# Kernel optimization log

Hardware: AMD Instinct MI355X
Metric: run time of the kernel (lower is better)

Reference implementation:

```python
import jax, jax.numpy as jnp
import numpy as np

B, T, D, H = 2, 2048, 2048, 32
d = D // H  # head_dim = 64


def setup_inputs() -> dict:
    key = jax.random.key(0)
    ks = jax.random.split(key, 6)
    s = 2 ** (-2.5) * (2.0 / (D + D)) ** 0.5  # xavier_uniform-ish scale, gain 2^-2.5
    return {
        "hidden_states": jax.random.normal(ks[0], (B, T, D), jnp.float32),
        "Wq": jax.random.normal(ks[1], (D, D), jnp.float32) * s,
        "Wk": jax.random.normal(ks[2], (D, D), jnp.float32) * s,
        "Wv": jax.random.normal(ks[3], (D, D), jnp.float32) * s,
        "Wbeta": jax.random.normal(ks[4], (D, H), jnp.float32) * s,
        "b_beta": jnp.zeros((H,), jnp.float32),
        "Wo": jax.random.normal(ks[5], (D, D), jnp.float32) * s,
    }


def _l2norm(x):
    return x * jax.lax.rsqrt(jnp.sum(x * x, axis=-1, keepdims=True) + 1e-6)


def _parallel_hope(q, k, v, beta):
    """Householder delta-rule linear attention.
    q,k,v: [B,H,T,d]; beta: [B,H,T].
    Recurrence: S_t = S_{t-1} (I - beta_t k_t k_t^T) + beta_t k_t v_t^T  (k l2-normalized,
    so the update is a generalized Householder transform), o_t = q_t^T S_t.
    """
    q = _l2norm(q)
    k = _l2norm(k)

    def step(S, inp):
        q_t, k_t, v_t, b_t = inp  # [B,H,d], [B,H,d], [B,H,d], [B,H]
        # delta rule: new value replaces old prediction, gated by beta
        pred = jnp.einsum('bhk,bhkv->bhv', k_t, S)
        delta = (v_t - pred) * b_t[..., None]
        S = S + jnp.einsum('bhk,bhv->bhkv', k_t, delta)
        o_t = jnp.einsum('bhk,bhkv->bhv', q_t, S)
        return S, o_t

    S0 = jnp.zeros(q.shape[:2] + (q.shape[-1], v.shape[-1]), q.dtype)  # [B,H,d,d]
    xs = (jnp.moveaxis(q, 2, 0), jnp.moveaxis(k, 2, 0),
          jnp.moveaxis(v, 2, 0), jnp.moveaxis(beta, 2, 0))
    _, o = jax.lax.scan(step, S0, xs)  # [T,B,H,d]
    return jnp.moveaxis(o, 0, 2)  # [B,H,T,d]


def reference(hidden_states, Wq, Wk, Wv, Wbeta, b_beta, Wo):
    q = hidden_states @ Wq
    k = hidden_states @ Wk
    v = hidden_states @ Wv
    beta = jax.nn.sigmoid(hidden_states @ Wbeta + b_beta)  # [B,T,H]
    to_heads = lambda x: jnp.moveaxis(x.reshape(B, T, H, d), 1, 2)  # [B,H,T,d]
    q, k, v = to_heads(q), to_heads(k), to_heads(v)
    beta = jnp.moveaxis(beta, 1, 2)  # [B,H,T]
    o = _parallel_hope(q, k, v, beta)  # [B,H,T,d]
    o = jnp.moveaxis(o, 1, 2).reshape(B, T, D)
    return o @ Wo
```

## Files before the change

### kernel.cpp

```cpp
#include <hip/hip_runtime.h>
#include <hip/hip_bf16.h>

typedef __hip_bfloat16 bf16;
typedef __attribute__((ext_vector_type(8))) short short8;
typedef __attribute__((ext_vector_type(4))) float f32x4;

#define NB 2
#define NT 2048
#define ND 2048
#define NH 32
#define NM (NB*NT)
#define NCH 32

__global__ void detect_dtype(const unsigned short* __restrict__ hs, int* __restrict__ flag) {
  if (threadIdx.x == 0 && blockIdx.x == 0) {
    int cnt = 0;
    for (int i = 0; i < 2048; i += 2) {
      int e = (hs[i] >> 7) & 0xFF;
      if (e >= 141) ++cnt;
    }
    *flag = (cnt > 64) ? 1 : 0;
  }
}

__device__ __forceinline__ float loadf(const void* p, size_t i, int isf32) {
  return isf32 ? ((const float*)p)[i] : __bfloat162float(((const bf16*)p)[i]);
}

__global__ __launch_bounds__(256) void convert_bf16(const void* __restrict__ src,
                                                    bf16* __restrict__ dst,
                                                    long n, const int* __restrict__ flag) {
  const long i0 = ((long)blockIdx.x * 256 + threadIdx.x) * 8;
  if (i0 >= n) return;
  if (*flag) {
    const float* s = (const float*)src;
    #pragma unroll
    for (int j = 0; j < 8; ++j) dst[i0 + j] = __float2bfloat16(s[i0 + j]);
  } else {
    *(short8*)(dst + i0) = *(const short8*)((const bf16*)src + i0);
  }
}

__global__ __launch_bounds__(256) void transpose_cvt(const void* __restrict__ src,
                                                     bf16* __restrict__ dst,
                                                     int src_rows, int src_cols,
                                                     const int* __restrict__ flag) {
  __shared__ bf16 tile[64][65];
  const int f = *flag;
  const int tb_r = blockIdx.y * 64, tb_c = blockIdx.x * 64;
  const int tx = threadIdx.x & 63, ty = threadIdx.x >> 6;
  #pragma unroll
  for (int i = 0; i < 64; i += 4) {
    const int cc = tb_c + tx;
    tile[i + ty][tx] = (cc < src_cols)
      ? __float2bfloat16(loadf(src, (size_t)(tb_r + i + ty) * src_cols + cc, f))
      : __float2bfloat16(0.f);
  }
  __syncthreads();
  #pragma unroll
  for (int i = 0; i < 64; i += 4)
    dst[(size_t)(tb_c + i + ty) * src_rows + tb_r + tx] = tile[tx][i + ty];
}

__global__ __launch_bounds__(256) void transpose_qkvb(const void* __restrict__ Wq,
                                                      const void* __restrict__ Wk,
                                                      const void* __restrict__ Wv,
                                                      const void* __restrict__ Wb,
                                                      bf16* __restrict__ WT,
                                                      const int* __restrict__ flag) {
  __shared__ bf16 tile[64][65];
  const int z = blockIdx.z;
  if (z == 3 && blockIdx.x >= 4) return;
  const void* src = (z == 0) ? Wq : (z == 1) ? Wk : (z == 2) ? Wv : Wb;
  const int src_cols = (z == 3) ? 32 : 2048;
  bf16* dst = WT + (size_t)z * 2048 * 2048;
  const int f = *flag;
  const int tb_r = blockIdx.y * 64, tb_c = blockIdx.x * 64;
  const int tx = threadIdx.x & 63, ty = threadIdx.x >> 6;
  #pragma unroll
  for (int i = 0; i < 64; i += 4) {
    const int cc = tb_c + tx;
    tile[i + ty][tx] = (cc < src_cols)
      ? __float2bfloat16(loadf(src, (size_t)(tb_r + i + ty) * src_cols + cc, f))
      : __float2bfloat16(0.f);
  }
  __syncthreads();
  #pragma unroll
  for (int i = 0; i < 64; i += 4)
    dst[(size_t)(tb_c + i + ty) * 2048 + tb_r + tx] = tile[tx][i + ty];
}

__device__ __forceinline__ void gload_lds16(const void* g, void* l) {
  __builtin_amdgcn_global_load_lds((__attribute__((address_space(1))) const void*)g,
                                   (__attribute__((address_space(3))) void*)l,
                                   16, 0, 0);
}

__global__ __launch_bounds__(256) void gemm_bt(const bf16* __restrict__ A,
                                               const bf16* __restrict__ Bt,
                                               bf16* __restrict__ oq, bf16* __restrict__ ok2,
                                               bf16* __restrict__ ov, bf16* __restrict__ ob,
                                               void* __restrict__ outv,
                                               const int* __restrict__ outflag,
                                               int M, int K, int n_base) {
  __shared__ bf16 As[128 * 32];
  __shared__ bf16 Bs[128 * 32];
  const int tid = threadIdx.x;
  const int wave = tid >> 6, lane = tid & 63;
  const int m0 = blockIdx.y * 128, n0 = blockIdx.x * 128;
  const int wm = (wave >> 1) * 64, wn = (wave & 1) * 64;
  const int srow = lane >> 2, scol = (lane & 3) * 8;
  const int frow = lane & 15, fk = (lane >> 4) * 8;
  f32x4 acc[4][4] = {};

  for (int kb = 0; kb < K; kb += 32) {
    __syncthreads();
    #pragma unroll
    for (int j = 0; j < 2; ++j) {
      const int rbase = wave * 32 + j * 16;
      gload_lds16(A  + (size_t)(m0 + rbase + srow) * K + kb + scol, As + rbase * 32);
      gload_lds16(Bt + (size_t)(n0 + rbase + srow) * K + kb + scol, Bs + rbase * 32);
    }
    __syncthreads();
    short8 af[4], bfr[4];
    #pragma unroll
    for (int i = 0; i < 4; ++i)
      af[i] = *(const short8*)(As + (wm + i * 16 + frow) * 32 + fk);
    #pragma unroll
    for (int i = 0; i < 4; ++i)
      bfr[i] = *(const short8*)(Bs + (wn + i * 16 + frow) * 32 + fk);
    #pragma unroll
    for (int mi = 0; mi < 4; ++mi)
      #pragma unroll
      for (int ni = 0; ni < 4; ++ni)
        acc[mi][ni] = __builtin_amdgcn_mfma_f32_16x16x32_bf16(af[mi], bfr[ni], acc[mi][ni], 0, 0, 0);
  }

  const int crow = (lane >> 4) * 4, ccol = lane & 15;
  const int gn0 = n_base + n0;
  if (outflag) {
    const int f = *outflag;
    #pragma unroll
    for (int mi = 0; mi < 4; ++mi)
      #pragma unroll
      for (int ni = 0; ni < 4; ++ni)
        #pragma unroll
        for (int r = 0; r < 4; ++r) {
          const size_t idx = (size_t)(m0 + wm + mi * 16 + crow + r) * 2048 + gn0 + wn + ni * 16 + ccol;
          const float val = acc[mi][ni][r];
          if (f == 1) ((float*)outv)[idx] = val;
          else        ((bf16*)outv)[idx] = __float2bfloat16(val);
        }
  } else {
    const int seg = gn0 >> 11;
    bf16* o = (seg == 0) ? oq : (seg == 1) ? ok2 : (seg == 2) ? ov : ob;
    const int stride = (seg < 3) ? 2048 : 128;
    const int cb = (gn0 & 2047) + wn;
    if (seg <= 1) {
      #pragma unroll
      for (int mi = 0; mi < 4; ++mi)
        #pragma unroll
        for (int r = 0; r < 4; ++r) {
          float s = acc[mi][0][r] * acc[mi][0][r] + acc[mi][1][r] * acc[mi][1][r]
                  + acc[mi][2][r] * acc[mi][2][r] + acc[mi][3][r] * acc[mi][3][r];
          s += __shfl_xor(s, 1, 64); s += __shfl_xor(s, 2, 64);
          s += __shfl_xor(s, 4, 64); s += __shfl_xor(s, 8, 64);
          const float inv = rsqrtf(s + 1e-6f);
          #pragma unroll
          for (int ni = 0; ni < 4; ++ni) acc[mi][ni][r] *= inv;
        }
    }
    #pragma unroll
    for (int mi = 0; mi < 4; ++mi)
      #pragma unroll
      for (int ni = 0; ni < 4; ++ni)
        #pragma unroll
        for (int r = 0; r < 4; ++r)
          o[(size_t)(m0 + wm + mi * 16 + crow + r) * stride + cb + ni * 16 + ccol] =
            __float2bfloat16(acc[mi][ni][r]);
  }
}


#define MFMA_PAIR(P)                                                             \
  _Pragma("unroll") for (int q2 = 0; q2 < 2; ++q2)                               \
    _Pragma("unroll") for (int ni2 = 0; ni2 < 4; ++ni2) {                        \
      acc[(P) * 2 + q2][ni2] = __builtin_amdgcn_mfma_f32_16x16x32_bf16(          \
          aF[q2][0], bF[ni2][0], acc[(P) * 2 + q2][ni2], 0, 0, 0);               \
      acc[(P) * 2 + q2][ni2] = __builtin_amdgcn_mfma_f32_16x16x32_bf16(          \
          aF[q2][1], bF[ni2][1], acc[(P) * 2 + q2][ni2], 0, 0, 0);               \
    }

#define READ_A(P)                                                                \
  _Pragma("unroll") for (int q2 = 0; q2 < 2; ++q2)                               \
    _Pragma("unroll") for (int kk = 0; kk < 2; ++kk)                             \
      aF[q2][kk] = *(const short8*)(lA + (((P) * 2 + q2) * 16 + frow) * 128      \
                                       + ((kk * 64 + fq * 16) ^ fswz));

#define READ_B_ALL()                                                             \
  _Pragma("unroll") for (int ni2 = 0; ni2 < 4; ++ni2)                            \
    _Pragma("unroll") for (int kk = 0; kk < 2; ++kk)                             \
      bF[ni2][kk] = *(const short8*)(lB + (brow0 + ni2 * 16 + frow) * 128        \
                                        + ((kk * 64 + fq * 16) ^ fswz));

#define PH_OPEN() do { __builtin_amdgcn_s_barrier();                             \
  asm volatile("s_waitcnt lgkmcnt(0)" ::: "memory");                             \
  __builtin_amdgcn_sched_barrier(0);                                             \
  __builtin_amdgcn_s_setprio(1); } while (0)

#define PH_CLOSE() do { __builtin_amdgcn_s_setprio(0);                           \
  __builtin_amdgcn_s_barrier(); } while (0)

__global__ __launch_bounds__(512, 2) void gemm256(const bf16* __restrict__ A,
                                                  const bf16* __restrict__ Bt,
                                                  bf16* __restrict__ oq, bf16* __restrict__ ok2,
                                                  bf16* __restrict__ ov, bf16* __restrict__ ob,
                                                  void* __restrict__ outv,
                                                  const int* __restrict__ outflag,
                                                  int K, int ntn) {
  __shared__ bf16 LA[2][2][8192];
  __shared__ bf16 LB[2][2][8192];
  const int tid = threadIdx.x;
  const int wave = tid >> 6, lane = tid & 63;
  const int wm = wave >> 2, wn = wave & 3;
  const int frow = lane & 15, fq = lane >> 4;
  const int cpx = (int)gridDim.x >> 3;
  const int wg = ((int)blockIdx.x & 7) * cpx + ((int)blockIdx.x >> 3);
  const int mtile = wg / ntn, ntile = wg % ntn;
  const int m0 = mtile * 256, n0 = ntile * 256;
  const int NTK = K >> 6;
  const int fswz = (frow & 7) << 4;
  int srow[2], scolb[2];
  #pragma unroll
  for (int j = 0; j < 2; ++j) {
    const int q = wave * 1024 + j * 8192 + lane * 16;
    const int qs = q ^ (((q >> 7) & 7) << 4);
    srow[j]  = qs >> 7;
    scolb[j] = (qs & 127) >> 1;
  }
  const int lofs = wave * 1024;

  f32x4 acc[8][4] = {};

  auto STAGE = [&](const bf16* __restrict__ G, int row0, int kcol, bf16* lhalf) {
    #pragma unroll
    for (int j = 0; j < 2; ++j)
      gload_lds16(G + (size_t)(row0 + srow[j]) * K + kcol + scolb[j],
                  (char*)lhalf + lofs + j * 8192);
  };

  STAGE(A,  m0,       0,  LA[0][0]);
  STAGE(A,  m0 + 128, 0,  LA[0][1]);
  STAGE(Bt, n0,       0,  LB[0][0]);
  STAGE(Bt, n0 + 128, 0,  LB[0][1]);
  STAGE(A,  m0,       64, LA[1][0]);
  STAGE(A,  m0 + 128, 64, LA[1][1]);
  asm volatile("s_waitcnt vmcnt(4)" ::: "memory");
  __builtin_amdgcn_s_barrier();

  const int brow0 = (wn & 1) * 64;
  #pragma unroll 1
  for (int t = 0; t < NTK; ++t) {
    const int par = t & 1;
    const char* lA = (const char*)LA[par][wm];
    const char* lB = (const char*)LB[par][wn >> 1];
    short8 aF[2][2], bF[4][2];
    READ_A(0)
    READ_B_ALL()
    if (t + 1 < NTK) STAGE(Bt, n0, (t + 1) * 64, LB[par ^ 1][0]);
    PH_OPEN();
    MFMA_PAIR(0)
    PH_CLOSE();
    READ_A(1)
    if (t + 1 < NTK) STAGE(Bt, n0 + 128, (t + 1) * 64, LB[par ^ 1][1]);
    PH_OPEN();
    MFMA_PAIR(1)
    PH_CLOSE();
    READ_A(2)
    PH_OPEN();
    MFMA_PAIR(2)
    PH_CLOSE();
    READ_A(3)
    PH_OPEN();
    MFMA_PAIR(3)
    __builtin_amdgcn_s_setprio(0);
    __builtin_amdgcn_s_barrier();
    if (t + 1 < NTK) {
      if (t + 2 < NTK) {
        STAGE(A, m0,       (t + 2) * 64, LA[par][0]);
        STAGE(A, m0 + 128, (t + 2) * 64, LA[par][1]);
      }
      if (t == NTK - 2) asm volatile("s_waitcnt vmcnt(0)" ::: "memory");
      else              asm volatile("s_waitcnt vmcnt(4)" ::: "memory");
      __builtin_amdgcn_s_barrier();
    }
  }

  const int crow = fq * 4, ccol = frow;
  const int rowb = m0 + wm * 128;
  if (outv) {
    const int f = *outflag;
    const int cb = n0 + wn * 64;
    #pragma unroll
    for (int mi = 0; mi < 8; ++mi)
      #pragma unroll
      for (int ni = 0; ni < 4; ++ni)
        #pragma unroll
        for (int r = 0; r < 4; ++r) {
          const size_t idx = (size_t)(rowb + mi * 16 + crow + r) * 2048 + cb + ni * 16 + ccol;
          const float val = acc[mi][ni][r];
          if (f == 1) ((float*)outv)[idx] = val;
          else        ((bf16*)outv)[idx] = __float2bfloat16(val);
        }
    return;
  }
  const int gn0w = n0 + wn * 64;
  const int seg = gn0w >> 11;
  bf16* o = (seg == 0) ? oq : (seg == 1) ? ok2 : (seg == 2) ? ov : ob;
  const int stride = (seg < 3) ? 2048 : 256;
  const int cb = (seg < 3) ? (gn0w & 2047) : (gn0w - 6144);
  if (seg <= 1) {
    #pragma unroll
    for (int mi = 0; mi < 8; ++mi)
      #pragma unroll
      for (int r = 0; r < 4; ++r) {
        float s = acc[mi][0][r] * acc[mi][0][r] + acc[mi][1][r] * acc[mi][1][r]
                + acc[mi][2][r] * acc[mi][2][r] + acc[mi][3][r] * acc[mi][3][r];
        s += __shfl_xor(s, 1, 64); s += __shfl_xor(s, 2, 64);
        s += __shfl_xor(s, 4, 64); s += __shfl_xor(s, 8, 64);
        const float inv = rsqrtf(s + 1e-6f);
        #pragma unroll
        for (int ni = 0; ni < 4; ++ni) acc[mi][ni][r] *= inv;
      }
  }
  #pragma unroll
  for (int mi = 0; mi < 8; ++mi)
    #pragma unroll
    for (int ni = 0; ni < 4; ++ni)
      #pragma unroll
      for (int r = 0; r < 4; ++r)
        o[(size_t)(rowb + mi * 16 + crow + r) * stride + cb + ni * 16 + ccol] =
          __float2bfloat16(acc[mi][ni][r]);
}


template<int TB>
__device__ __forceinline__ void scan16(const float* __restrict__ Af,
                                       const bf16* __restrict__ vsrc,
                                       const float* __restrict__ Bsc,
                                       float (&u)[64], const int lane, const int wave,
                                       const float sgn,
                                       bf16* __restrict__ outT,
                                       bf16* __restrict__ gout) {
  constexpr int JM = (TB + 1) * 16;
  #pragma unroll
  for (int tt = 0; tt < 16; ++tt) {
    const int t = TB * 16 + tt;
    float pr0 = 0.f, pr1 = 0.f, pr2 = 0.f, pr3 = 0.f;
    #pragma unroll
    for (int i = 0; i < JM; i += 4) {
      const f32x4 a = *(const f32x4*)(Af + t * 64 + i);
      pr0 = __builtin_fmaf(a[0], u[i + 0], pr0);
      pr1 = __builtin_fmaf(a[1], u[i + 1], pr1);
      pr2 = __builtin_fmaf(a[2], u[i + 2], pr2);
      pr3 = __builtin_fmaf(a[3], u[i + 3], pr3);
    }
    const float ut = Bsc[t] * __bfloat162float(vsrc[t * 72 + lane])
                   - ((pr0 + pr1) + (pr2 + pr3));
    u[t] = ut;
    const bf16 sv = __float2bfloat16(sgn * ut);
    outT[lane * 72 + t] = sv;
    if (wave) gout[t * 64 + lane] = sv;
  }
}

__global__ __launch_bounds__(256) void chunk_scan(const bf16* __restrict__ k16,
                                                  bf16* __restrict__ v16,
                                                  const bf16* __restrict__ betab,
                                                  const void* __restrict__ bb,
                                                  const int* __restrict__ flag,
                                                  bf16* __restrict__ Gneg,
                                                  bf16* __restrict__ AcT,
                                                  bf16* __restrict__ Dc) {
  __shared__ bf16 Ks[64 * 72];
  __shared__ bf16 Vs[64 * 72];
  __shared__ bf16 GsT[64 * 72];
  __shared__ bf16 UsT[64 * 72];
  __shared__ float Af[64 * 64];
  __shared__ float Bsc[64];
  bf16* const KTs = (bf16*)Af;
  const int ch = blockIdx.x;
  const int c = ch & (NCH - 1), bh = ch >> 5;
  const int h = bh & (NH - 1), b = bh >> 5;
  const int tid = threadIdx.x, wave = tid >> 6, lane = tid & 63;
  const size_t rowb = ((size_t)b * NT + c * 64) * ND + (size_t)h * 64;

  short8 ktA0, ktB0, ktA1, ktB1;
  if (wave >= 2) {
    const int d0a = (wave - 2) * 16, d0b = d0a + 32;
    ktA0 = *(const short8*)(k16 + rowb + (size_t)lane * ND + d0a);
    ktB0 = *(const short8*)(k16 + rowb + (size_t)lane * ND + d0a + 8);
    ktA1 = *(const short8*)(k16 + rowb + (size_t)lane * ND + d0b);
    ktB1 = *(const short8*)(k16 + rowb + (size_t)lane * ND + d0b + 8);
  }
  {
    const int r0 = tid >> 3, sc = (tid & 7) * 8;
    #pragma unroll
    for (int rnd = 0; rnd < 2; ++rnd) {
      const int r = rnd * 32 + r0;
      *(short8*)(Ks + r * 72 + sc) = *(const short8*)(k16 + rowb + (size_t)r * ND + sc);
      *(short8*)(Vs + r * 72 + sc) = *(const short8*)(v16 + rowb + (size_t)r * ND + sc);
    }
  }
  if (tid < 64) {
    const float x = __bfloat162float(betab[((size_t)b * NT + c * 64 + tid) * 256 + h])
                    + loadf(bb, h, *flag);
    Bsc[tid] = 1.f / (1.f + expf(-x));
  }
  __syncthreads();

  const int frow = lane & 15, fk = (lane >> 4) * 8, cm = (lane >> 4) * 4;
  {
    short8 ma0 = *(const short8*)(Ks + (16 * wave + frow) * 72 + fk);
    short8 ma1 = *(const short8*)(Ks + (16 * wave + frow) * 72 + 32 + fk);
    #pragma unroll
    for (int n = 0; n < 4; ++n) {
      f32x4 m = {};
      m = __builtin_amdgcn_mfma_f32_16x16x32_bf16(ma0, *(const short8*)(Ks + (16 * n + frow) * 72 + fk), m, 0, 0, 0);
      m = __builtin_amdgcn_mfma_f32_16x16x32_bf16(ma1, *(const short8*)(Ks + (16 * n + frow) * 72 + 32 + fk), m, 0, 0, 0);
      #pragma unroll
      for (int r = 0; r < 4; ++r) {
        const int t = 16 * wave + cm + r, s = 16 * n + frow;
        Af[t * 64 + s] = (s < t) ? Bsc[t] * m[r] : 0.f;
      }
    }
  }
  __syncthreads();

  if (wave < 2) {
    float u[64];
    #pragma unroll
    for (int i = 0; i < 64; ++i) u[i] = 0.f;
    const bf16* vsrc = wave ? Ks : Vs;
    bf16* outT = wave ? GsT : UsT;
    bf16* gout = Gneg + (size_t)ch * 4096;
    const float sgn = wave ? -1.f : 1.f;
    scan16<0>(Af, vsrc, Bsc, u, lane, wave, sgn, outT, gout);
    scan16<1>(Af, vsrc, Bsc, u, lane, wave, sgn, outT, gout);
    scan16<2>(Af, vsrc, Bsc, u, lane, wave, sgn, outT, gout);
    scan16<3>(Af, vsrc, Bsc, u, lane, wave, sgn, outT, gout);
  }
  __syncthreads();

  if (wave >= 2) {
    const int d0a = (wave - 2) * 16, d0b = d0a + 32;
    #pragma unroll
    for (int j = 0; j < 8; ++j) {
      KTs[(d0a + j) * 72 + lane]     = ((const bf16*)&ktA0)[j];
      KTs[(d0a + 8 + j) * 72 + lane] = ((const bf16*)&ktB0)[j];
      KTs[(d0b + j) * 72 + lane]     = ((const bf16*)&ktA1)[j];
      KTs[(d0b + 8 + j) * 72 + lane] = ((const bf16*)&ktB1)[j];
    }
  }
  __syncthreads();

  short8 ka0 = *(const short8*)(KTs + (16 * wave + frow) * 72 + fk);
  short8 ka1 = *(const short8*)(KTs + (16 * wave + frow) * 72 + 32 + fk);
  short8 uu0 = *(const short8*)(UsT + (16 * wave + frow) * 72 + fk);
  short8 uu1 = *(const short8*)(UsT + (16 * wave + frow) * 72 + 32 + fk);
  #pragma unroll
  for (int n = 0; n < 4; ++n) {
    f32x4 aA = {}, aD = {};
    aA = __builtin_amdgcn_mfma_f32_16x16x32_bf16(ka0, *(const short8*)(GsT + (16 * n + frow) * 72 + fk), aA, 0, 0, 0);
    aA = __builtin_amdgcn_mfma_f32_16x16x32_bf16(ka1, *(const short8*)(GsT + (16 * n + frow) * 72 + 32 + fk), aA, 0, 0, 0);
    aD = __builtin_amdgcn_mfma_f32_16x16x32_bf16(uu0, *(const short8*)(KTs + (16 * n + frow) * 72 + fk), aD, 0, 0, 0);
    aD = __builtin_amdgcn_mfma_f32_16x16x32_bf16(uu1, *(const short8*)(KTs + (16 * n + frow) * 72 + 32 + fk), aD, 0, 0, 0);
    #pragma unroll
    for (int r = 0; r < 4; ++r) {
      Vs[(16 * wave + cm + r) * 64 + 16 * n + frow] = __float2bfloat16(aA[r]);
      Ks[(16 * wave + cm + r) * 64 + 16 * n + frow] = __float2bfloat16(aD[r]);
    }
  }
  __syncthreads();
  {
    const int r0 = tid >> 2, sc2 = (tid & 3) * 16;
    bf16* acg = AcT + (size_t)ch * 4096;
    bf16* dcg = Dc  + (size_t)ch * 4096;
    *(short8*)(acg + r0 * 64 + sc2)     = *(const short8*)(Vs + r0 * 64 + sc2);
    *(short8*)(acg + r0 * 64 + sc2 + 8) = *(const short8*)(Vs + r0 * 64 + sc2 + 8);
    *(short8*)(dcg + r0 * 64 + sc2)     = *(const short8*)(Ks + r0 * 64 + sc2);
    *(short8*)(dcg + r0 * 64 + sc2 + 8) = *(const short8*)(Ks + r0 * 64 + sc2 + 8);
    *(short8*)(v16 + rowb + (size_t)r0 * ND + sc2)     = *(const short8*)(UsT + r0 * 72 + sc2);
    *(short8*)(v16 + rowb + (size_t)r0 * ND + sc2 + 8) = *(const short8*)(UsT + r0 * 72 + sc2 + 8);
  }
}

__global__ __launch_bounds__(256) void state_seq(const bf16* __restrict__ AcT,
                                                 const bf16* __restrict__ Dc,
                                                 bf16* __restrict__ Sbuf) {
  __shared__ bf16 ST[64 * 72];
  const int bh = blockIdx.x;
  const int wave = threadIdx.x >> 6, lane = threadIdx.x & 63;
  const int frow = lane & 15, fk = (lane >> 4) * 8, cm = (lane >> 4) * 4;
  for (int i = threadIdx.x; i < 64 * 72 / 2; i += 256) ((unsigned int*)ST)[i] = 0u;
  f32x4 sacc[4] = {};
  const bf16* ac = AcT + (size_t)bh * NCH * 4096;
  const bf16* dc = Dc  + (size_t)bh * NCH * 4096;
  bf16* sb = Sbuf + (size_t)bh * NCH * 4096;
  #pragma unroll
  for (int n = 0; n < 4; ++n)
    #pragma unroll
    for (int r = 0; r < 4; ++r)
      sb[(16 * wave + cm + r) * 64 + 16 * n + frow] = __float2bfloat16(0.f);
  short8 bpre[4][2];
  float dpre[16];
  #pragma unroll
  for (int n = 0; n < 4; ++n) {
    bpre[n][0] = *(const short8*)(ac + (16 * n + frow) * 64 + fk);
    bpre[n][1] = *(const short8*)(ac + (16 * n + frow) * 64 + 32 + fk);
    #pragma unroll
    for (int r = 0; r < 4; ++r)
      dpre[n * 4 + r] = __bfloat162float(dc[(16 * wave + cm + r) * 64 + 16 * n + frow]);
  }
  __syncthreads();
  #pragma unroll 1
  for (int c = 0; c < NCH; ++c) {
    short8 a0 = *(const short8*)(ST + (16 * wave + frow) * 72 + fk);
    short8 a1 = *(const short8*)(ST + (16 * wave + frow) * 72 + 32 + fk);
    short8 bcur[4][2];
    float dcur[16];
    #pragma unroll
    for (int n = 0; n < 4; ++n) {
      bcur[n][0] = bpre[n][0]; bcur[n][1] = bpre[n][1];
      #pragma unroll
      for (int r = 0; r < 4; ++r) dcur[n * 4 + r] = dpre[n * 4 + r];
    }
    if (c + 1 < NCH) {
      const bf16* acn = ac + (size_t)(c + 1) * 4096;
      const bf16* dcn = dc + (size_t)(c + 1) * 4096;
      #pragma unroll
      for (int n = 0; n < 4; ++n) {
        bpre[n][0] = *(const short8*)(acn + (16 * n + frow) * 64 + fk);
        bpre[n][1] = *(const short8*)(acn + (16 * n + frow) * 64 + 32 + fk);
        #pragma unroll
        for (int r = 0; r < 4; ++r)
          dpre[n * 4 + r] = __bfloat162float(dcn[(16 * wave + cm + r) * 64 + 16 * n + frow]);
      }
    }
    #pragma unroll
    for (int n = 0; n < 4; ++n) {
      sacc[n] = __builtin_amdgcn_mfma_f32_16x16x32_bf16(a0, bcur[n][0], sacc[n], 0, 0, 0);
      sacc[n] = __builtin_amdgcn_mfma_f32_16x16x32_bf16(a1, bcur[n][1], sacc[n], 0, 0, 0);
      #pragma unroll
      for (int r = 0; r < 4; ++r) sacc[n][r] += dcur[n * 4 + r];
    }
    __syncthreads();
    #pragma unroll
    for (int n = 0; n < 4; ++n)
      #pragma unroll
      for (int r = 0; r < 4; ++r) {
        const bf16 sv = __float2bfloat16(sacc[n][r]);
        ST[(16 * wave + cm + r) * 72 + 16 * n + frow] = sv;
        if (c + 1 < NCH)
          sb[(size_t)(c + 1) * 4096 + (16 * wave + cm + r) * 64 + 16 * n + frow] = sv;
      }
    __syncthreads();
  }
}

__global__ __launch_bounds__(256) void chunk_out(bf16* __restrict__ q16,
                                                 const bf16* __restrict__ k16,
                                                 const bf16* __restrict__ v16,
                                                 const bf16* __restrict__ Gneg,
                                                 const bf16* __restrict__ Sbuf) {
  __shared__ bf16 UTs[64 * 72];
  __shared__ bf16 Pt[64 * 72];
  const int ch = blockIdx.x;
  const int c = ch & (NCH - 1), bh = ch >> 5;
  const int h = bh & (NH - 1), b = bh >> 5;
  const int tid = threadIdx.x, wave = tid >> 6, lane = tid & 63;
  const int frow = lane & 15, fk = (lane >> 4) * 8, cm = (lane >> 4) * 4;
  const size_t qkb = ((size_t)b * NT + c * 64) * ND + (size_t)h * 64;
  const bf16* Sb = Sbuf + (size_t)ch * 4096;
  const bf16* Gc = Gneg + (size_t)ch * 4096;
  {
    const int r0 = tid >> 2, sc2 = (tid & 3) * 16;
    *(short8*)(UTs + r0 * 72 + sc2)     = *(const short8*)(v16 + qkb + (size_t)r0 * ND + sc2);
    *(short8*)(UTs + r0 * 72 + sc2 + 8) = *(const short8*)(v16 + qkb + (size_t)r0 * ND + sc2 + 8);
  }
  short8 qa0 = *(const short8*)(q16 + qkb + (size_t)(16 * wave + frow) * ND + fk);
  short8 qa1 = *(const short8*)(q16 + qkb + (size_t)(16 * wave + frow) * ND + 32 + fk);
  f32x4 pacc[4];
  #pragma unroll
  for (int n = 0; n < 4; ++n) {
    f32x4 a = {};
    a = __builtin_amdgcn_mfma_f32_16x16x32_bf16(qa0, *(const short8*)(k16 + qkb + (size_t)(16 * n + frow) * ND + fk), a, 0, 0, 0);
    a = __builtin_amdgcn_mfma_f32_16x16x32_bf16(qa1, *(const short8*)(k16 + qkb + (size_t)(16 * n + frow) * ND + 32 + fk), a, 0, 0, 0);
    pacc[n] = a;
  }
  __syncthreads();
  f32x4 uacc[4];
  #pragma unroll
  for (int n = 0; n < 4; ++n)
    #pragma unroll
    for (int r = 0; r < 4; ++r)
      uacc[n][r] = __bfloat162float(UTs[(16 * wave + cm + r) * 72 + 16 * n + frow]);
  #pragma unroll
  for (int n = 0; n < 4; ++n)
    #pragma unroll
    for (int r = 0; r < 4; ++r) {
      const int mg = 16 * wave + cm + r, ng = 16 * n + frow;
      Pt[mg * 72 + ng] = __float2bfloat16(ng <= mg ? pacc[n][r] : 0.f);
    }
  short8 sa0 = *(const short8*)(Sb + (16 * wave + frow) * 64 + fk);
  short8 sa1 = *(const short8*)(Sb + (16 * wave + frow) * 64 + 32 + fk);
  #pragma unroll
  for (int n = 0; n < 4; ++n) {
    uacc[n] = __builtin_amdgcn_mfma_f32_16x16x32_bf16(sa0, *(const short8*)(Gc + (16 * n + frow) * 64 + fk), uacc[n], 0, 0, 0);
    uacc[n] = __builtin_amdgcn_mfma_f32_16x16x32_bf16(sa1, *(const short8*)(Gc + (16 * n + frow) * 64 + 32 + fk), uacc[n], 0, 0, 0);
  }
  __syncthreads();
  #pragma unroll
  for (int n = 0; n < 4; ++n)
    #pragma unroll
    for (int r = 0; r < 4; ++r)
      UTs[(16 * wave + cm + r) * 72 + 16 * n + frow] = __float2bfloat16(uacc[n][r]);
  __syncthreads();
  short8 pa0 = *(const short8*)(Pt + (16 * wave + frow) * 72 + fk);
  short8 pa1 = *(const short8*)(Pt + (16 * wave + frow) * 72 + 32 + fk);
  #pragma unroll
  for (int n = 0; n < 4; ++n) {
    f32x4 o = {};
    o = __builtin_amdgcn_mfma_f32_16x16x32_bf16(qa0, *(const short8*)(Sb + (16 * n + frow) * 64 + fk), o, 0, 0, 0);
    o = __builtin_amdgcn_mfma_f32_16x16x32_bf16(qa1, *(const short8*)(Sb + (16 * n + frow) * 64 + 32 + fk), o, 0, 0, 0);
    o = __builtin_amdgcn_mfma_f32_16x16x32_bf16(pa0, *(const short8*)(UTs + (16 * n + frow) * 72 + fk), o, 0, 0, 0);
    o = __builtin_amdgcn_mfma_f32_16x16x32_bf16(pa1, *(const short8*)(UTs + (16 * n + frow) * 72 + 32 + fk), o, 0, 0, 0);
    #pragma unroll
    for (int r = 0; r < 4; ++r)
      q16[qkb + (size_t)(16 * wave + cm + r) * ND + 16 * n + frow] = __float2bfloat16(o[r]);
  }
}


__global__ __launch_bounds__(128) void chunk_scan_c(const bf16* __restrict__ k16,
                                                    bf16* __restrict__ v16,
                                                    const bf16* __restrict__ betab,
                                                    const void* __restrict__ bb,
                                                    const int* __restrict__ flag,
                                                    bf16* __restrict__ Gneg) {
  __shared__ bf16 Ks[64 * 64];
  __shared__ bf16 Vs[64 * 64];
  __shared__ bf16 Gs[64 * 64];
  __shared__ float Bs[64];
  const int ch = blockIdx.x;
  const int c = ch & (NCH - 1), bh = ch >> 5;
  const int h = bh & (NH - 1), b = bh >> 5;
  const int tid = threadIdx.x;
  const int wave = tid >> 6, lane = tid & 63;
  const size_t rowb = ((size_t)b * NT + c * 64) * ND + (size_t)h * 64;
  const int sr = tid >> 3, sc = (tid & 7) * 8;
  #pragma unroll
  for (int rnd = 0; rnd < 4; ++rnd) {
    const int r = rnd * 16 + sr;
    *(short8*)(Ks + r * 64 + sc) = *(const short8*)(k16 + rowb + (size_t)r * ND + sc);
    *(short8*)(Vs + r * 64 + sc) = *(const short8*)(v16 + rowb + (size_t)r * ND + sc);
  }
  if (tid < 64) {
    const float x = __bfloat162float(betab[((size_t)b * NT + c * 64 + tid) * 128 + h])
                    + loadf(bb, h, *flag);
    Bs[tid] = 1.f / (1.f + expf(-x));
  }
  __syncthreads();
  float S[64];
  #pragma unroll
  for (int i = 0; i < 64; ++i) S[i] = 0.f;
  const bf16* val_src = wave ? Ks : Vs;
  #pragma unroll 1
  for (int t = 0; t < 64; ++t) {
    uint4 ku[8];
    #pragma unroll
    for (int i = 0; i < 8; ++i) ku[i] = ((const uint4*)(Ks + t * 64))[i];
    const float val = __bfloat162float(val_src[t * 64 + lane]);
    const float bt = Bs[t];
    float kvf[64];
    #pragma unroll
    for (int i = 0; i < 8; ++i) {
      kvf[8*i+0] = __uint_as_float(ku[i].x << 16);
      kvf[8*i+1] = __uint_as_float(ku[i].x & 0xffff0000u);
      kvf[8*i+2] = __uint_as_float(ku[i].y << 16);
      kvf[8*i+3] = __uint_as_float(ku[i].y & 0xffff0000u);
      kvf[8*i+4] = __uint_as_float(ku[i].z << 16);
      kvf[8*i+5] = __uint_as_float(ku[i].z & 0xffff0000u);
      kvf[8*i+6] = __uint_as_float(ku[i].w << 16);
      kvf[8*i+7] = __uint_as_float(ku[i].w & 0xffff0000u);
    }
    float p0 = 0, p1 = 0, p2 = 0, p3 = 0;
    #pragma unroll
    for (int i = 0; i < 16; ++i) {
      p0 += kvf[4*i+0] * S[4*i+0];
      p1 += kvf[4*i+1] * S[4*i+1];
      p2 += kvf[4*i+2] * S[4*i+2];
      p3 += kvf[4*i+3] * S[4*i+3];
    }
    const float u = bt * (val - ((p0 + p1) + (p2 + p3)));
    #pragma unroll
    for (int i = 0; i < 16; ++i) {
      S[4*i+0] += kvf[4*i+0] * u;
      S[4*i+1] += kvf[4*i+1] * u;
      S[4*i+2] += kvf[4*i+2] * u;
      S[4*i+3] += kvf[4*i+3] * u;
    }
    if (wave) Gs[t * 64 + lane] = __float2bfloat16(-u);
    else      Vs[t * 64 + lane] = __float2bfloat16(u);
  }
  __syncthreads();
  bf16* gout = Gneg + (size_t)ch * 4096;
  #pragma unroll
  for (int rnd = 0; rnd < 4; ++rnd) {
    const int r = rnd * 16 + sr;
    *(short8*)(v16 + rowb + (size_t)r * ND + sc) = *(const short8*)(Vs + r * 64 + sc);
    *(short8*)(gout + r * 64 + sc)               = *(const short8*)(Gs + r * 64 + sc);
  }
}

__global__ __launch_bounds__(256) void chunk_seq_mono(bf16* q16,
                                                      const bf16* __restrict__ k16,
                                                      const bf16* __restrict__ Ul,
                                                      const bf16* __restrict__ Gneg) {
  __shared__ bf16 ST[64 * 72];
  __shared__ bf16 Ubt[64 * 72];
  __shared__ bf16 Pt[64 * 72];
  __shared__ bf16 KTl[64 * 72];
  const int bh = blockIdx.x, h = bh & (NH - 1), b = bh >> 5;
  const int wave = threadIdx.x >> 6, lane = threadIdx.x & 63;
  const int frow = lane & 15, q4 = lane >> 4, fk = q4 * 8;
  const int cm = q4 * 4;
  for (int i = threadIdx.x; i < 64 * 72 / 2; i += 256) ((unsigned int*)ST)[i] = 0u;
  __syncthreads();
  f32x4 sacc[4] = {};
  #pragma unroll 1
  for (int c = 0; c < NCH; ++c) {
    const bf16* Gc = Gneg + ((size_t)bh * NCH + c) * 4096;
    const size_t qkb = ((size_t)b * NT + c * 64) * ND + (size_t)h * 64;
    {
      short8 r0 = *(const short8*)(k16 + qkb + (size_t)lane * ND + 16 * wave);
      short8 r1 = *(const short8*)(k16 + qkb + (size_t)lane * ND + 16 * wave + 8);
      #pragma unroll
      for (int j = 0; j < 8; ++j) {
        KTl[(16 * wave + j) * 72 + lane]     = ((const bf16*)&r0)[j];
        KTl[(16 * wave + 8 + j) * 72 + lane] = ((const bf16*)&r1)[j];
      }
    }
    short8 ga0 = *(const short8*)(Gc + (16 * wave + frow) * 64 + fk);
    short8 ga1 = *(const short8*)(Gc + (16 * wave + frow) * 64 + 32 + fk);
    #pragma unroll
    for (int n = 0; n < 4; ++n) {
      f32x4 acc;
      #pragma unroll
      for (int r = 0; r < 4; ++r)
        acc[r] = __bfloat162float(Ul[qkb + (size_t)(16 * wave + cm + r) * ND + 16 * n + frow]);
      acc = __builtin_amdgcn_mfma_f32_16x16x32_bf16(ga0, *(const short8*)(ST + (16 * n + frow) * 72 + fk), acc, 0, 0, 0);
      acc = __builtin_amdgcn_mfma_f32_16x16x32_bf16(ga1, *(const short8*)(ST + (16 * n + frow) * 72 + 32 + fk), acc, 0, 0, 0);
      #pragma unroll
      for (int r = 0; r < 4; ++r)
        Ubt[(16 * n + frow) * 72 + 16 * wave + cm + r] = __float2bfloat16(acc[r]);
    }
    __syncthreads();
    short8 qa0 = *(const short8*)(q16 + qkb + (size_t)(16 * wave + frow) * ND + fk);
    short8 qa1 = *(const short8*)(q16 + qkb + (size_t)(16 * wave + frow) * ND + 32 + fk);
    #pragma unroll
    for (int n = 0; n < 4; ++n) {
      f32x4 acc = {};
      acc = __builtin_amdgcn_mfma_f32_16x16x32_bf16(qa0, *(const short8*)(k16 + qkb + (size_t)(16 * n + frow) * ND + fk), acc, 0, 0, 0);
      acc = __builtin_amdgcn_mfma_f32_16x16x32_bf16(qa1, *(const short8*)(k16 + qkb + (size_t)(16 * n + frow) * ND + 32 + fk), acc, 0, 0, 0);
      #pragma unroll
      for (int r = 0; r < 4; ++r) {
        const int mg = 16 * wave + cm + r, ng = 16 * n + frow;
        Pt[mg * 72 + ng] = __float2bfloat16(ng <= mg ? acc[r] : 0.f);
      }
    }
    __syncthreads();
    short8 pa0 = *(const short8*)(Pt + (16 * wave + frow) * 72 + fk);
    short8 pa1 = *(const short8*)(Pt + (16 * wave + frow) * 72 + 32 + fk);
    #pragma unroll
    for (int n = 0; n < 4; ++n) {
      f32x4 acc = {};
      acc = __builtin_amdgcn_mfma_f32_16x16x32_bf16(qa0, *(const short8*)(ST + (16 * n + frow) * 72 + fk), acc, 0, 0, 0);
      acc = __builtin_amdgcn_mfma_f32_16x16x32_bf16(qa1, *(const short8*)(ST + (16 * n + frow) * 72 + 32 + fk), acc, 0, 0, 0);
      acc = __builtin_amdgcn_mfma_f32_16x16x32_bf16(pa0, *(const short8*)(Ubt + (16 * n + frow) * 72 + fk), acc, 0, 0, 0);
      acc = __builtin_amdgcn_mfma_f32_16x16x32_bf16(pa1, *(const short8*)(Ubt + (16 * n + frow) * 72 + 32 + fk), acc, 0, 0, 0);
      #pragma unroll
      for (int r = 0; r < 4; ++r)
        q16[qkb + (size_t)(16 * wave + cm + r) * ND + 16 * n + frow] = __float2bfloat16(acc[r]);
    }
    __syncthreads();
    short8 ua0 = *(const short8*)(Ubt + (16 * wave + frow) * 72 + fk);
    short8 ua1 = *(const short8*)(Ubt + (16 * wave + frow) * 72 + 32 + fk);
    #pragma unroll
    for (int n = 0; n < 4; ++n) {
      sacc[n] = __builtin_amdgcn_mfma_f32_16x16x32_bf16(ua0, *(const short8*)(KTl + (16 * n + frow) * 72 + fk), sacc[n], 0, 0, 0);
      sacc[n] = __builtin_amdgcn_mfma_f32_16x16x32_bf16(ua1, *(const short8*)(KTl + (16 * n + frow) * 72 + 32 + fk), sacc[n], 0, 0, 0);
      #pragma unroll
      for (int r = 0; r < 4; ++r)
        ST[(16 * wave + cm + r) * 72 + 16 * n + frow] = __float2bfloat16(sacc[n][r]);
    }
    __syncthreads();
  }
}

extern "C" void kernel_launch(void* const* d_in, const int* in_sizes, int n_in,
                              void* d_out, int out_size, void* d_ws, size_t ws_size,
                              hipStream_t stream) {
  const void* hs = d_in[0];
  const void* Wq = d_in[1];
  const void* Wk = d_in[2];
  const void* Wv = d_in[3];
  const void* Wb = d_in[4];
  const void* bb = d_in[5];
  const void* Wo = d_in[6];

  char* ws = (char*)d_ws;
  size_t off = 0;
  auto alloc = [&](size_t bytes) {
    void* p = ws + off;
    off += (bytes + 255) & ~(size_t)255;
    return p;
  };
  const size_t szW2 = (size_t)32 * 1024 * 1024;
  const size_t szM  = (size_t)NM * ND * 2;
  const size_t szB2 = (size_t)NM * 256 * 2;
  const size_t szB  = (size_t)NM * 128 * 2;
  const size_t need_fused = 512 + szW2 + 4 * szM + szB2 + szM;

  if (ws_size >= need_fused) {
    int*  flag  = (int*) alloc(256);
    bf16* WT    = (bf16*)alloc(szW2);
    bf16* hs16  = (bf16*)alloc(szM);
    bf16* q16   = (bf16*)alloc(szM);
    bf16* k16   = (bf16*)alloc(szM);
    bf16* v16   = (bf16*)alloc(szM);
    bf16* betab = (bf16*)alloc(szB2);
    bf16* Dc    = (bf16*)alloc(szM);
    bf16* Gneg  = WT;
    bf16* AcT   = WT + (size_t)8 * 1024 * 1024;
    bf16* WoT   = AcT;
    bf16* Sbuf  = hs16;

    detect_dtype<<<1, 64, 0, stream>>>((const unsigned short*)hs, flag);
    convert_bf16<<<(NM * ND) / (256 * 8), 256, 0, stream>>>(hs, hs16, (long)NM * ND, flag);

    transpose_qkvb<<<dim3(32, 32, 4), 256, 0, stream>>>(Wq, Wk, Wv, Wb, WT, flag);
    gemm256<<<400, 512, 0, stream>>>(hs16, WT, q16, k16, v16, betab,
                                     nullptr, nullptr, ND, 25);

    chunk_scan<<<NB * NH * NCH, 256, 0, stream>>>(k16, v16, betab, bb, flag, Gneg, AcT, Dc);
    state_seq<<<NB * NH, 256, 0, stream>>>(AcT, Dc, Sbuf);
    chunk_out<<<NB * NH * NCH, 256, 0, stream>>>(q16, k16, v16, Gneg, Sbuf);

    transpose_cvt<<<dim3(32, 32), 256, 0, stream>>>(Wo, WoT, 2048, 2048, flag);
    gemm256<<<128, 512, 0, stream>>>(q16, WoT, nullptr, nullptr, nullptr, nullptr,
                                     d_out, flag, ND, 8);
  } else {
    int*  flag  = (int*) alloc(256);
    bf16* Wt    = (bf16*)alloc((size_t)2048 * 2048 * 2);
    bf16* hs16  = (bf16*)alloc(szM);
    bf16* q16   = (bf16*)alloc(szM);
    bf16* k16   = (bf16*)alloc(szM);
    bf16* v16   = (bf16*)alloc(szM);
    bf16* betab = (bf16*)alloc(szB);
    bf16* Gneg  = hs16;

    detect_dtype<<<1, 64, 0, stream>>>((const unsigned short*)hs, flag);
    convert_bf16<<<(NM * ND) / (256 * 8), 256, 0, stream>>>(hs, hs16, (long)NM * ND, flag);

    transpose_cvt<<<dim3(32, 32), 256, 0, stream>>>(Wq, Wt, 2048, 2048, flag);
    gemm_bt<<<dim3(16, 32), 256, 0, stream>>>(hs16, Wt, q16, k16, v16, betab, nullptr, nullptr, NM, ND, 0);
    transpose_cvt<<<dim3(32, 32), 256, 0, stream>>>(Wk, Wt, 2048, 2048, flag);
    gemm_bt<<<dim3(16, 32), 256, 0, stream>>>(hs16, Wt, q16, k16, v16, betab, nullptr, nullptr, NM, ND, 2048);
    transpose_cvt<<<dim3(32, 32), 256, 0, stream>>>(Wv, Wt, 2048, 2048, flag);
    gemm_bt<<<dim3(16, 32), 256, 0, stream>>>(hs16, Wt, q16, k16, v16, betab, nullptr, nullptr, NM, ND, 4096);
    transpose_cvt<<<dim3(2, 32),  256, 0, stream>>>(Wb, Wt, 2048, 32, flag);
    gemm_bt<<<dim3(1, 32), 256, 0, stream>>>(hs16, Wt, q16, k16, v16, betab, nullptr, nullptr, NM, ND, 6144);

    chunk_scan_c<<<NB * NH * NCH, 128, 0, stream>>>(k16, v16, betab, bb, flag, Gneg);
    chunk_seq_mono<<<NB * NH, 256, 0, stream>>>(q16, k16, v16, Gneg);

    transpose_cvt<<<dim3(32, 32), 256, 0, stream>>>(Wo, Wt, 2048, 2048, flag);
    gemm_bt<<<dim3(16, 32), 256, 0, stream>>>(q16, Wt, nullptr, nullptr, nullptr, nullptr,
                                              d_out, flag, NM, ND, 0);
  }
}
```

Before: 581.8 us.

## Double-buffer A fragments in gemm256 and route output projection to gemm_bt

The main-loop LDS reads in gemm256 become ping-pong fragment buffers. The next A fragment pair is read while the current MFMA phase runs, with a partial lgkmcnt wait, and the first fragments of the next K-tile are prefetched after the barrier. This is meant to hide LDS read latency behind the matrix ops. Separately, the output projection now uses the gemm_bt kernel with a 16x32 grid instead of the 128-block gemm256 launch, aiming for better CU occupancy on the smaller GEMM. Both raise register pressure and change which kernel handles the final write.

```diff
diff --git a/kernel.cpp b/kernel.cpp
--- a/kernel.cpp
+++ b/kernel.cpp
@@ -182,29 +182,29 @@
 }
 
 
-#define MFMA_PAIR(P)                                                             \
-  _Pragma("unroll") for (int q2 = 0; q2 < 2; ++q2)                               \
-    _Pragma("unroll") for (int ni2 = 0; ni2 < 4; ++ni2) {                        \
-      acc[(P) * 2 + q2][ni2] = __builtin_amdgcn_mfma_f32_16x16x32_bf16(          \
-          aF[q2][0], bF[ni2][0], acc[(P) * 2 + q2][ni2], 0, 0, 0);               \
-      acc[(P) * 2 + q2][ni2] = __builtin_amdgcn_mfma_f32_16x16x32_bf16(          \
-          aF[q2][1], bF[ni2][1], acc[(P) * 2 + q2][ni2], 0, 0, 0);               \
-    }
-
-#define READ_A(P)                                                                \
+#define READ_PAIR(DST, P)                                                        \
   _Pragma("unroll") for (int q2 = 0; q2 < 2; ++q2)                               \
     _Pragma("unroll") for (int kk = 0; kk < 2; ++kk)                             \
-      aF[q2][kk] = *(const short8*)(lA + (((P) * 2 + q2) * 16 + frow) * 128      \
-                                       + ((kk * 64 + fq * 16) ^ fswz));
-
-#define READ_B_ALL()                                                             \
+      DST[q2][kk] = *(const short8*)(lA + (((P) * 2 + q2) * 16 + frow) * 128     \
+                                        + ((kk * 64 + fq * 16) ^ fswz));
+
+#define READ_BALL()                                                              \
   _Pragma("unroll") for (int ni2 = 0; ni2 < 4; ++ni2)                            \
     _Pragma("unroll") for (int kk = 0; kk < 2; ++kk)                             \
       bF[ni2][kk] = *(const short8*)(lB + (brow0 + ni2 * 16 + frow) * 128        \
                                         + ((kk * 64 + fq * 16) ^ fswz));
 
-#define PH_OPEN() do { __builtin_amdgcn_s_barrier();                             \
-  asm volatile("s_waitcnt lgkmcnt(0)" ::: "memory");                             \
+#define MFMA_P(SRC, P)                                                           \
+  _Pragma("unroll") for (int q2 = 0; q2 < 2; ++q2)                               \
+    _Pragma("unroll") for (int ni2 = 0; ni2 < 4; ++ni2) {                        \
+      acc[(P) * 2 + q2][ni2] = __builtin_amdgcn_mfma_f32_16x16x32_bf16(          \
+          SRC[q2][0], bF[ni2][0], acc[(P) * 2 + q2][ni2], 0, 0, 0);              \
+      acc[(P) * 2 + q2][ni2] = __builtin_amdgcn_mfma_f32_16x16x32_bf16(          \
+          SRC[q2][1], bF[ni2][1], acc[(P) * 2 + q2][ni2], 0, 0, 0);              \
+    }
+
+#define PH_OPEN_CNT(N) do { __builtin_amdgcn_s_barrier();                        \
+  asm volatile("s_waitcnt lgkmcnt(" #N ")" ::: "memory");                        \
   __builtin_amdgcn_sched_barrier(0);                                             \
   __builtin_amdgcn_s_setprio(1); } while (0)
 
@@ -241,6 +241,7 @@
   const int lofs = wave * 1024;
 
   f32x4 acc[8][4] = {};
+  short8 aFA[2][2], aFB[2][2], bF[4][2];
 
   auto STAGE = [&](const bf16* __restrict__ G, int row0, int kcol, bf16* lhalf) {
     #pragma unroll
@@ -259,30 +260,35 @@
   __builtin_amdgcn_s_barrier();
 
   const int brow0 = (wn & 1) * 64;
+  {
+    const char* lA = (const char*)LA[0][wm];
+    const char* lB = (const char*)LB[0][wn >> 1];
+    READ_PAIR(aFA, 0)
+    READ_BALL()
+    __builtin_amdgcn_sched_barrier(0);
+  }
+
   #pragma unroll 1
   for (int t = 0; t < NTK; ++t) {
     const int par = t & 1;
     const char* lA = (const char*)LA[par][wm];
     const char* lB = (const char*)LB[par][wn >> 1];
-    short8 aF[2][2], bF[4][2];
-    READ_A(0)
-    READ_B_ALL()
+    READ_PAIR(aFB, 1)
     if (t + 1 < NTK) STAGE(Bt, n0, (t + 1) * 64, LB[par ^ 1][0]);
-    PH_OPEN();
-    MFMA_PAIR(0)
+    PH_OPEN_CNT(4);
+    MFMA_P(aFA, 0)
     PH_CLOSE();
-    READ_A(1)
+    READ_PAIR(aFA, 2)
     if (t + 1 < NTK) STAGE(Bt, n0 + 128, (t + 1) * 64, LB[par ^ 1][1]);
-    PH_OPEN();
-    MFMA_PAIR(1)
+    PH_OPEN_CNT(4);
+    MFMA_P(aFB, 1)
     PH_CLOSE();
-    READ_A(2)
-    PH_OPEN();
-    MFMA_PAIR(2)
+    READ_PAIR(aFB, 3)
+    PH_OPEN_CNT(4);
+    MFMA_P(aFA, 2)
     PH_CLOSE();
-    READ_A(3)
-    PH_OPEN();
-    MFMA_PAIR(3)
+    PH_OPEN_CNT(0);
+    MFMA_P(aFB, 3)
     __builtin_amdgcn_s_setprio(0);
     __builtin_amdgcn_s_barrier();
     if (t + 1 < NTK) {
@@ -293,6 +299,15 @@
       if (t == NTK - 2) asm volatile("s_waitcnt vmcnt(0)" ::: "memory");
       else              asm volatile("s_waitcnt vmcnt(4)" ::: "memory");
       __builtin_amdgcn_s_barrier();
+      {
+        const char* lAn = (const char*)LA[par ^ 1][wm];
+        const char* lBn = (const char*)LB[par ^ 1][wn >> 1];
+        const char* lA = lAn;
+        const char* lB = lBn;
+        READ_PAIR(aFA, 0)
+        READ_BALL()
+        __builtin_amdgcn_sched_barrier(0);
+      }
     }
   }
 
@@ -858,8 +873,8 @@
     chunk_out<<<NB * NH * NCH, 256, 0, stream>>>(q16, k16, v16, Gneg, Sbuf);
 
     transpose_cvt<<<dim3(32, 32), 256, 0, stream>>>(Wo, WoT, 2048, 2048, flag);
-    gemm256<<<128, 512, 0, stream>>>(q16, WoT, nullptr, nullptr, nullptr, nullptr,
-                                     d_out, flag, ND, 8);
+    gemm_bt<<<dim3(16, 32), 256, 0, stream>>>(q16, WoT, nullptr, nullptr, nullptr, nullptr,
+                                              d_out, flag, NM, ND, 0);
   } else {
     int*  flag  = (int*) alloc(256);
     bf16* Wt    = (bf16*)alloc((size_t)2048 * 2048 * 2);
```

After: 574.0 us. Within noise of the previous version (-1.3%).
